# Kernel tuning notes

Measured on AMD Instinct MI355X. Metric: run time of the kernel, lower is better.

The kernel has to match this reference:

```python
import jax, jax.numpy as jnp
import numpy as np

B, L, D, H = 64, 1024, 2048, 128
BUDGET = 10       # args.ceg_budget
STEP = 0.01       # args.ceg_step_size
EPS = 0.2         # _pgd_search default eps


def setup_inputs() -> dict:
    key = jax.random.key(0)
    k0, k1, k2 = jax.random.split(key, 3)
    x = jax.random.normal(k0, (B, L, D), dtype=jnp.float32)
    W1 = jax.random.normal(k1, (D, H), dtype=jnp.float32) * (1.0 / np.sqrt(D))
    b1 = jnp.zeros((H,), dtype=jnp.float32)
    W2 = jax.random.normal(k2, (H, 1), dtype=jnp.float32) * (1.0 / np.sqrt(H))
    b2 = jnp.zeros((1,), dtype=jnp.float32)
    return {"x": x, "W1": W1, "b1": b1, "W2": W2, "b2": b2}


def _score(xa, W1, b1, W2, b2):
    # property_scorer: Linear -> GELU(exact erf, torch default) -> Linear -> Sigmoid
    h = jax.nn.gelu(xa @ W1 + b1, approximate=False)   # [B, H]
    return jax.nn.sigmoid(h @ W2 + b2)                  # [B, 1]


def reference(x, W1, b1, W2, b2):
    pooled = x.mean(axis=1)                             # [B, D]
    # x_adv = pooled + randn * 0.01 (fixed key for determinism)
    noise = jax.random.normal(jax.random.key(1), pooled.shape, pooled.dtype)
    x_adv0 = pooled + 0.01 * noise

    grad_fn = jax.grad(lambda xa: _score(xa, W1, b1, W2, b2).sum())

    def pgd_step(x_adv, _):
        g = jnp.sign(grad_fn(x_adv))
        x_adv = x_adv - STEP * g
        delta = jnp.clip(x_adv - pooled, -EPS, EPS)
        return pooled + delta, None

    x_adv, _ = jax.lax.scan(pgd_step, x_adv0, None, length=BUDGET)

    worst_score = _score(x_adv, W1, b1, W2, b2).squeeze(-1)  # [B]
    violated = worst_score.min() < 0.1                        # scalar bool
    cert_score = 1.0 - worst_score                            # [B]
    return x, worst_score, cert_score, violated
```

## Files before the change

kernel.cpp:

```cpp
#include <hip/hip_runtime.h>
#include <hip/hip_bf16.h>
#include <stdint.h>

#define DEV __device__ __forceinline__

typedef float f32x4 __attribute__((ext_vector_type(4)));

constexpr int nB = 64;
constexpr int nL = 1024;
constexpr int nD = 2048;
constexpr int nH = 128;

constexpr int NT = 16;
constexpr int LT = nL / NT;

constexpr size_t X_ELEMS = (size_t)nB * (size_t)nL * (size_t)nD;

DEV float gelu_f(float x) {
  return 0.5f * x * (1.0f + erff(x * 0.7071067811865476f));
}
DEV float gelu_grad_f(float x) {
  return 0.5f * (1.0f + erff(x * 0.7071067811865476f))
       + x * 0.3989422804014327f * expf(-0.5f * x * x);
}
DEV float sigmoid_f(float x) { return 1.0f / (1.0f + expf(-x)); }

DEV uint32_t rotl32(uint32_t v, int r) { return (v << r) | (v >> (32 - r)); }

DEV float bf2f(uint16_t u) { return __uint_as_float(((uint32_t)u) << 16); }

DEV void threefry_key01(uint32_t& x0, uint32_t& x1) {
  const uint32_t ks0 = 0u, ks1 = 1u, ks2 = 0x1BD11BDAu ^ 0u ^ 1u;
  x0 += ks0; x1 += ks1;
#define TF_RND(r) { x0 += x1; x1 = rotl32(x1, (r)); x1 ^= x0; }
  TF_RND(13) TF_RND(15) TF_RND(26) TF_RND(6)
  x0 += ks1; x1 += ks2 + 1u;
  TF_RND(17) TF_RND(29) TF_RND(16) TF_RND(24)
  x0 += ks2; x1 += ks0 + 2u;
  TF_RND(13) TF_RND(15) TF_RND(26) TF_RND(6)
  x0 += ks0; x1 += ks1 + 3u;
  TF_RND(17) TF_RND(29) TF_RND(16) TF_RND(24)
  x0 += ks1; x1 += ks2 + 4u;
  TF_RND(13) TF_RND(15) TF_RND(26) TF_RND(6)
  x0 += ks2; x1 += ks0 + 5u;
#undef TF_RND
}

DEV float erfinv_f32(float x) {
  float w = -log1pf(-x * x);
  float p;
  if (w < 5.0f) {
    w -= 2.5f;
    p = 2.81022636e-08f;
    p = fmaf(p, w, 3.43273939e-07f);
    p = fmaf(p, w, -3.5233877e-06f);
    p = fmaf(p, w, -4.39150654e-06f);
    p = fmaf(p, w, 0.00021858087f);
    p = fmaf(p, w, -0.00125372503f);
    p = fmaf(p, w, -0.00417768164f);
    p = fmaf(p, w, 0.246640727f);
    p = fmaf(p, w, 1.50140941f);
  } else {
    w = sqrtf(w) - 3.0f;
    p = -0.000200214257f;
    p = fmaf(p, w, 0.000100950558f);
    p = fmaf(p, w, 0.00134934322f);
    p = fmaf(p, w, -0.00367342844f);
    p = fmaf(p, w, 0.00573950773f);
    p = fmaf(p, w, -0.0076224613f);
    p = fmaf(p, w, 0.00943887047f);
    p = fmaf(p, w, 1.00167406f);
    p = fmaf(p, w, 2.83297682f);
  }
  return p * x;
}

DEV float jax_normal_key1(int i) {
  const uint32_t j = (uint32_t)(i & 0xFFFF);
  uint32_t x0 = j, x1 = j + 65536u;
  threefry_key01(x0, x1);
  const uint32_t bits = (i < 65536) ? x0 : x1;
  const float u01 = __uint_as_float((bits >> 9) | 0x3F800000u) - 1.0f;
  const float lo = __uint_as_float(0xBF7FFFFFu);
  float v = u01 * 2.0f + lo;
  v = fmaxf(lo, v);
  return 1.4142135623730951f * erfinv_f32(v);
}

__global__ __launch_bounds__(256) void k_copy_mean(
    const float* __restrict__ x, float* __restrict__ out,
    float* __restrict__ pmean)
{
  const int blk = blockIdx.x;
  const int t = threadIdx.x;
  const size_t base = (size_t)blk * LT * nD;
  const size_t o0 = (size_t)4 * t;
  const size_t o1 = 1024 + (size_t)4 * t;
  f32x4 a0 = {0.f, 0.f, 0.f, 0.f};
  f32x4 a1 = {0.f, 0.f, 0.f, 0.f};
  for (int l = 0; l < LT; l += 2) {
    const size_t r0 = base + (size_t)l * nD;
    const size_t r1 = r0 + nD;
    const f32x4 v0 = *reinterpret_cast<const f32x4*>(x + r0 + o0);
    const f32x4 v1 = *reinterpret_cast<const f32x4*>(x + r0 + o1);
    const f32x4 u0 = *reinterpret_cast<const f32x4*>(x + r1 + o0);
    const f32x4 u1 = *reinterpret_cast<const f32x4*>(x + r1 + o1);
    *reinterpret_cast<f32x4*>(out + r0 + o0) = v0;
    *reinterpret_cast<f32x4*>(out + r0 + o1) = v1;
    *reinterpret_cast<f32x4*>(out + r1 + o0) = u0;
    *reinterpret_cast<f32x4*>(out + r1 + o1) = u1;
    a0 += v0; a1 += v1;
    a0 += u0; a1 += u1;
  }
  float* pm = pmean + (size_t)blk * nD;
  *reinterpret_cast<f32x4*>(pm + o0) = a0;
  *reinterpret_cast<f32x4*>(pm + o1) = a1;
}

__global__ __launch_bounds__(256) void k_copy_mean_atomic(
    const float* __restrict__ x, float* __restrict__ out,
    float* __restrict__ pooled)
{
  const int blk = blockIdx.x;
  const int b = blk >> 4;
  const int t = threadIdx.x;
  const size_t base = (size_t)blk * LT * nD;
  const size_t o0 = (size_t)4 * t;
  const size_t o1 = 1024 + (size_t)4 * t;
  f32x4 a0 = {0.f, 0.f, 0.f, 0.f};
  f32x4 a1 = {0.f, 0.f, 0.f, 0.f};
  for (int l = 0; l < LT; ++l) {
    const size_t r = base + (size_t)l * nD;
    const f32x4 v0 = *reinterpret_cast<const f32x4*>(x + r + o0);
    const f32x4 v1 = *reinterpret_cast<const f32x4*>(x + r + o1);
    *reinterpret_cast<f32x4*>(out + r + o0) = v0;
    *reinterpret_cast<f32x4*>(out + r + o1) = v1;
    a0 += v0; a1 += v1;
  }
  float* pp = pooled + (size_t)b * nD;
  const float sc = 1.0f / nL;
  atomicAdd(&pp[o0+0], a0.x*sc); atomicAdd(&pp[o0+1], a0.y*sc);
  atomicAdd(&pp[o0+2], a0.z*sc); atomicAdd(&pp[o0+3], a0.w*sc);
  atomicAdd(&pp[o1+0], a1.x*sc); atomicAdd(&pp[o1+1], a1.y*sc);
  atomicAdd(&pp[o1+2], a1.z*sc); atomicAdd(&pp[o1+3], a1.w*sc);
}

__global__ __launch_bounds__(256) void k_prep(
    const float* __restrict__ W1, uint16_t* __restrict__ W1b,
    uint16_t* __restrict__ W1Tb)
{
  __shared__ float tile[64][65];
  const int bd = blockIdx.x;
  const int bh = blockIdx.y;
  const int t = threadIdx.x;
  const int j = t & 63;
  const int i0 = (t >> 6) * 16;
  for (int ii = 0; ii < 16; ++ii) {
    const int i = i0 + ii;
    const float v = W1[(size_t)(bd * 64 + i) * nH + bh * 64 + j];
    tile[i][j] = v;
    const __hip_bfloat16 hb = __float2bfloat16(v);
    W1b[(size_t)(bd * 64 + i) * nH + bh * 64 + j] =
        *reinterpret_cast<const uint16_t*>(&hb);
  }
  __syncthreads();
  for (int ii = 0; ii < 16; ++ii) {
    const int i = i0 + ii;
    const __hip_bfloat16 hb = __float2bfloat16(tile[j][i]);
    W1Tb[(size_t)(bh * 64 + i) * nD + bd * 64 + j] =
        *reinterpret_cast<const uint16_t*>(&hb);
  }
}

__global__ __launch_bounds__(1024) void k_pgd(
    const float* __restrict__ W1, const uint16_t* __restrict__ W1b,
    const uint16_t* __restrict__ W1Tb,
    const float* __restrict__ b1, const float* __restrict__ W2,
    const float* __restrict__ b2, const float* __restrict__ pmean,
    const float* __restrict__ pooledG, float* __restrict__ scores,
    const int from_partial)
{
  __shared__ float xaS[nD];
  __shared__ float pooledS[nD];
  __shared__ float redS[16][nH];
  __shared__ float dz1S[nH];
  __shared__ float red2[2];

  const int t = threadIdx.x;
  const int b = blockIdx.x;

  {
    float2 pl;
    if (from_partial) {
      float2 s = make_float2(0.f, 0.f);
      for (int nt2 = 0; nt2 < NT; ++nt2) {
        const float2 v = *reinterpret_cast<const float2*>(
            &pmean[((size_t)(b * NT + nt2)) * nD + 2 * t]);
        s.x += v.x; s.y += v.y;
      }
      pl = make_float2(s.x * (1.0f / nL), s.y * (1.0f / nL));
    } else {
      pl = *reinterpret_cast<const float2*>(&pooledG[(size_t)b * nD + 2 * t]);
    }
    pooledS[2 * t]     = pl.x;
    pooledS[2 * t + 1] = pl.y;
    const int i0 = b * nD + 2 * t;
    xaS[2 * t]     = pl.x + 0.01f * jax_normal_key1(i0);
    xaS[2 * t + 1] = pl.y + 0.01f * jax_normal_key1(i0 + 1);
  }

  const float b1t = (t < nH) ? b1[t] : 0.f;
  const float w2t = (t < nH) ? W2[t] : 0.f;
  const float b2s = b2[0];

  __syncthreads();

  const int hp = t & 63;
  const int q  = t >> 6;
  const uint32_t* __restrict__ w1b2 =
      reinterpret_cast<const uint32_t*>(W1b);
  const uint32_t* __restrict__ w1tb2 =
      reinterpret_cast<const uint32_t*>(W1Tb);
  const int hf = t & (nH - 1);
  const int dq = t >> 7;

  float sig_last = 0.f;
  for (int it = 0; it <= 10; ++it) {
    float z1 = 0.f;
    if (it < 10) {
      float accx = 0.f, accy = 0.f;
      const int dbase = q * 128;
      #pragma unroll 8
      for (int dd = 0; dd < 128; ++dd) {
        const float xv = xaS[dbase + dd];
        const uint32_t w = w1b2[(size_t)(dbase + dd) * 64 + hp];
        accx = fmaf(xv, bf2f((uint16_t)(w & 0xFFFF)), accx);
        accy = fmaf(xv, bf2f((uint16_t)(w >> 16)), accy);
      }
      redS[q][2 * hp]     = accx;
      redS[q][2 * hp + 1] = accy;
      __syncthreads();
      if (t < nH) {
        #pragma unroll
        for (int q2 = 0; q2 < 16; ++q2) z1 += redS[q2][t];
        z1 += b1t;
      }
    } else {
      float acc = 0.f;
      const float* __restrict__ w1p = W1 + (size_t)(dq * 256) * nH + hf;
      #pragma unroll 8
      for (int d = 0; d < 256; ++d)
        acc = fmaf(xaS[dq * 256 + d], w1p[(size_t)d * nH], acc);
      redS[dq][hf] = acc;
      __syncthreads();
      if (t < nH) {
        #pragma unroll
        for (int q2 = 0; q2 < 8; ++q2) z1 += redS[q2][t];
        z1 += b1t;
      }
    }

    if (t < nH) {
      float part = gelu_f(z1) * w2t;
      #pragma unroll
      for (int m = 1; m <= 32; m <<= 1) part += __shfl_xor(part, m, 64);
      if ((t & 63) == 0) red2[t >> 6] = part;
    }
    __syncthreads();

    const float sig = sigmoid_f(red2[0] + red2[1] + b2s);
    if (it == 10) { sig_last = sig; break; }

    if (t < nH) dz1S[t] = sig * (1.f - sig) * w2t * gelu_grad_f(z1);
    __syncthreads();

    float gx = 0.f, gy = 0.f;
    #pragma unroll 8
    for (int h = 0; h < nH; ++h) {
      const float dz = dz1S[h];
      const uint32_t w = w1tb2[(size_t)h * 1024 + t];
      gx = fmaf(dz, bf2f((uint16_t)(w & 0xFFFF)), gx);
      gy = fmaf(dz, bf2f((uint16_t)(w >> 16)), gy);
    }
    const float sg0 = (gx > 0.f) ? 1.f : ((gx < 0.f) ? -1.f : 0.f);
    const float sg1 = (gy > 0.f) ? 1.f : ((gy < 0.f) ? -1.f : 0.f);
    const float p0 = pooledS[2 * t], p1 = pooledS[2 * t + 1];
    float d0 = fminf(fmaxf((xaS[2 * t]     - 0.01f * sg0) - p0, -0.2f), 0.2f);
    float d1 = fminf(fmaxf((xaS[2 * t + 1] - 0.01f * sg1) - p1, -0.2f), 0.2f);
    xaS[2 * t]     = p0 + d0;
    xaS[2 * t + 1] = p1 + d1;
    __syncthreads();
  }

  if (t == 0) scores[b] = sig_last;
}

__global__ __launch_bounds__(256) void k_zero(float* __restrict__ p, int n) {
  const int i = blockIdx.x * 256 + threadIdx.x;
  if (i < n) p[i] = 0.f;
}

__global__ __launch_bounds__(64) void k_finalize(
    const float* __restrict__ scores, float* __restrict__ out)
{
  const int t = threadIdx.x;
  const float s = scores[t];
  out[X_ELEMS + t] = s;
  out[X_ELEMS + nB + t] = 1.0f - s;
  float m = s;
  for (int o = 32; o > 0; o >>= 1) m = fminf(m, __shfl_xor(m, o, 64));
  if (t == 0) out[X_ELEMS + 2 * nB] = (m < 0.1f) ? 1.0f : 0.0f;
}

extern "C" void kernel_launch(void* const* d_in, const int* in_sizes, int n_in,
                              void* d_out, int out_size, void* d_ws, size_t ws_size,
                              hipStream_t stream) {
  const float* x  = (const float*)d_in[0];
  const float* W1 = (const float*)d_in[1];
  const float* b1 = (const float*)d_in[2];
  const float* W2 = (const float*)d_in[3];
  const float* b2 = (const float*)d_in[4];
  float* out = (float*)d_out;
  float* ws = (float*)d_ws;

  constexpr size_t PMEAN_ELEMS  = (size_t)nB * NT * nD;
  constexpr size_t POOLED_ELEMS = (size_t)nB * nD;
  constexpr size_t W1_ELEMS     = (size_t)nD * nH;
  const size_t primary_bytes =
      PMEAN_ELEMS * 4 + W1_ELEMS * 2 * 2 + nB * 4;

  if (ws_size >= primary_bytes) {
    float*    pmean  = ws;
    uint16_t* w1b    = (uint16_t*)(ws + PMEAN_ELEMS);
    uint16_t* w1tb   = w1b + W1_ELEMS;
    float*    scores = (float*)(w1tb + W1_ELEMS);

    k_prep<<<dim3(32, 2), 256, 0, stream>>>(W1, w1b, w1tb);
    k_copy_mean<<<nB * NT, 256, 0, stream>>>(x, out, pmean);
    k_pgd<<<nB, 1024, 0, stream>>>(W1, w1b, w1tb, b1, W2, b2,
                                   pmean, nullptr, scores, 1);
    k_finalize<<<1, 64, 0, stream>>>(scores, out);
  } else {
    float*    pooled = ws;
    uint16_t* w1b    = (uint16_t*)(ws + POOLED_ELEMS);
    uint16_t* w1tb   = w1b + W1_ELEMS;
    float*    scores = (float*)(w1tb + W1_ELEMS);

    k_zero<<<(int)(POOLED_ELEMS + 255) / 256, 256, 0, stream>>>(
        pooled, (int)POOLED_ELEMS);
    k_prep<<<dim3(32, 2), 256, 0, stream>>>(W1, w1b, w1tb);
    k_copy_mean_atomic<<<nB * NT, 256, 0, stream>>>(x, out, pooled);
    k_pgd<<<nB, 1024, 0, stream>>>(W1, w1b, w1tb, b1, W2, b2,
                                   nullptr, pooled, scores, 0);
    k_finalize<<<1, 64, 0, stream>>>(scores, out);
  }
}
```

Baseline: 355.9 us.

## Fuse weight prep into copy kernel, finalize into PGD; widen PGD loads

```diff
diff --git a/kernel.cpp b/kernel.cpp
--- a/kernel.cpp
+++ b/kernel.cpp
@@ -5,6 +5,7 @@
 #define DEV __device__ __forceinline__
 
 typedef float f32x4 __attribute__((ext_vector_type(4)));
+typedef float f32x2 __attribute__((ext_vector_type(2)));
 
 constexpr int nB = 64;
 constexpr int nL = 1024;
@@ -27,7 +28,8 @@
 
 DEV uint32_t rotl32(uint32_t v, int r) { return (v << r) | (v >> (32 - r)); }
 
-DEV float bf2f(uint16_t u) { return __uint_as_float(((uint32_t)u) << 16); }
+DEV float bflo(uint32_t u) { return __uint_as_float(u << 16); }
+DEV float bfhi(uint32_t u) { return __uint_as_float(u & 0xFFFF0000u); }
 
 DEV void threefry_key01(uint32_t& x0, uint32_t& x1) {
   const uint32_t ks0 = 0u, ks1 = 1u, ks2 = 0x1BD11BDAu ^ 0u ^ 1u;
@@ -87,34 +89,247 @@
   return 1.4142135623730951f * erfinv_f32(v);
 }
 
-__global__ __launch_bounds__(256) void k_copy_mean(
+__global__ __launch_bounds__(256) void k_copy_prep(
     const float* __restrict__ x, float* __restrict__ out,
-    float* __restrict__ pmean)
+    float* __restrict__ pmean, const float* __restrict__ W1,
+    uint16_t* __restrict__ W1b, uint16_t* __restrict__ W1Tb,
+    int* __restrict__ ctr)
 {
+  __shared__ float tile[64][65];
+  const int t = threadIdx.x;
+
+  if (blockIdx.x >= (unsigned)(nB * NT)) {
+    const int pb = blockIdx.x - nB * NT;
+    const int bd = pb & 31;
+    const int bh = pb >> 5;
+    if (pb == 0 && t == 0) ctr[0] = 0;
+    const int j = t & 63;
+    const int i0 = (t >> 6) * 16;
+    for (int ii = 0; ii < 16; ++ii) {
+      const int i = i0 + ii;
+      const float v = W1[(size_t)(bd * 64 + i) * nH + bh * 64 + j];
+      tile[i][j] = v;
+      const __hip_bfloat16 hb = __float2bfloat16(v);
+      W1b[(size_t)(bd * 64 + i) * nH + bh * 64 + j] =
+          *reinterpret_cast<const uint16_t*>(&hb);
+    }
+    __syncthreads();
+    for (int ii = 0; ii < 16; ++ii) {
+      const int i = i0 + ii;
+      const __hip_bfloat16 hb = __float2bfloat16(tile[j][i]);
+      W1Tb[(size_t)(bh * 64 + i) * nD + bd * 64 + j] =
+          *reinterpret_cast<const uint16_t*>(&hb);
+    }
+    return;
+  }
+
   const int blk = blockIdx.x;
-  const int t = threadIdx.x;
   const size_t base = (size_t)blk * LT * nD;
   const size_t o0 = (size_t)4 * t;
   const size_t o1 = 1024 + (size_t)4 * t;
   f32x4 a0 = {0.f, 0.f, 0.f, 0.f};
   f32x4 a1 = {0.f, 0.f, 0.f, 0.f};
-  for (int l = 0; l < LT; l += 2) {
+  for (int l = 0; l < LT; l += 4) {
     const size_t r0 = base + (size_t)l * nD;
     const size_t r1 = r0 + nD;
+    const size_t r2 = r1 + nD;
+    const size_t r3 = r2 + nD;
     const f32x4 v0 = *reinterpret_cast<const f32x4*>(x + r0 + o0);
     const f32x4 v1 = *reinterpret_cast<const f32x4*>(x + r0 + o1);
-    const f32x4 u0 = *reinterpret_cast<const f32x4*>(x + r1 + o0);
-    const f32x4 u1 = *reinterpret_cast<const f32x4*>(x + r1 + o1);
+    const f32x4 v2 = *reinterpret_cast<const f32x4*>(x + r1 + o0);
+    const f32x4 v3 = *reinterpret_cast<const f32x4*>(x + r1 + o1);
+    const f32x4 v4 = *reinterpret_cast<const f32x4*>(x + r2 + o0);
+    const f32x4 v5 = *reinterpret_cast<const f32x4*>(x + r2 + o1);
+    const f32x4 v6 = *reinterpret_cast<const f32x4*>(x + r3 + o0);
+    const f32x4 v7 = *reinterpret_cast<const f32x4*>(x + r3 + o1);
     *reinterpret_cast<f32x4*>(out + r0 + o0) = v0;
     *reinterpret_cast<f32x4*>(out + r0 + o1) = v1;
-    *reinterpret_cast<f32x4*>(out + r1 + o0) = u0;
-    *reinterpret_cast<f32x4*>(out + r1 + o1) = u1;
+    *reinterpret_cast<f32x4*>(out + r1 + o0) = v2;
+    *reinterpret_cast<f32x4*>(out + r1 + o1) = v3;
+    *reinterpret_cast<f32x4*>(out + r2 + o0) = v4;
+    *reinterpret_cast<f32x4*>(out + r2 + o1) = v5;
+    *reinterpret_cast<f32x4*>(out + r3 + o0) = v6;
+    *reinterpret_cast<f32x4*>(out + r3 + o1) = v7;
     a0 += v0; a1 += v1;
-    a0 += u0; a1 += u1;
+    a0 += v2; a1 += v3;
+    a0 += v4; a1 += v5;
+    a0 += v6; a1 += v7;
   }
   float* pm = pmean + (size_t)blk * nD;
   *reinterpret_cast<f32x4*>(pm + o0) = a0;
   *reinterpret_cast<f32x4*>(pm + o1) = a1;
+}
+
+__global__ __launch_bounds__(1024) void k_pgd(
+    const float* __restrict__ W1, const uint16_t* __restrict__ W1b,
+    const uint16_t* __restrict__ W1Tb,
+    const float* __restrict__ b1, const float* __restrict__ W2,
+    const float* __restrict__ b2, const float* __restrict__ pmean,
+    const float* __restrict__ pooledG, float* __restrict__ scores,
+    int* __restrict__ ctr, float* __restrict__ out,
+    const int from_partial)
+{
+  __shared__ float xaS[nD];
+  __shared__ float pooledS[nD];
+  __shared__ float redS[32][nH];
+  __shared__ float redB[nD];
+  __shared__ float dz1S[nH];
+  __shared__ float red2[2];
+  __shared__ int lastS;
+
+  const int t = threadIdx.x;
+  const int b = blockIdx.x;
+
+  {
+    float2 pl;
+    if (from_partial) {
+      float2 s = make_float2(0.f, 0.f);
+      for (int nt2 = 0; nt2 < NT; ++nt2) {
+        const float2 v = *reinterpret_cast<const float2*>(
+            &pmean[((size_t)(b * NT + nt2)) * nD + 2 * t]);
+        s.x += v.x; s.y += v.y;
+      }
+      pl = make_float2(s.x * (1.0f / nL), s.y * (1.0f / nL));
+    } else {
+      pl = *reinterpret_cast<const float2*>(&pooledG[(size_t)b * nD + 2 * t]);
+    }
+    pooledS[2 * t]     = pl.x;
+    pooledS[2 * t + 1] = pl.y;
+    const int i0 = b * nD + 2 * t;
+    xaS[2 * t]     = pl.x + 0.01f * jax_normal_key1(i0);
+    xaS[2 * t + 1] = pl.y + 0.01f * jax_normal_key1(i0 + 1);
+  }
+
+  const float b1t = (t < nH) ? b1[t] : 0.f;
+  const float w2t = (t < nH) ? W2[t] : 0.f;
+  const float b2s = b2[0];
+
+  __syncthreads();
+
+  const int hq = t & 31;
+  const int c  = t >> 5;
+  const uint2* __restrict__ w1bq =
+      reinterpret_cast<const uint2*>(W1b);
+  const int dqd = t & 511;
+  const int hh  = t >> 9;
+  const uint2* __restrict__ w1tq =
+      reinterpret_cast<const uint2*>(W1Tb);
+  const int hf  = t & (nH - 1);
+  const int dq8 = t >> 7;
+
+  float sig_last = 0.f;
+  for (int it = 0; it <= 10; ++it) {
+    float z1 = 0.f;
+    if (it < 10) {
+      f32x2 a01 = {0.f, 0.f}, a23 = {0.f, 0.f};
+      const int dbase = c * 64;
+      #pragma unroll 4
+      for (int d4 = 0; d4 < 16; ++d4) {
+        const int d = dbase + d4 * 4;
+        const f32x4 xv4 = *reinterpret_cast<const f32x4*>(&xaS[d]);
+        #pragma unroll
+        for (int k = 0; k < 4; ++k) {
+          const uint2 w = w1bq[(size_t)(d + k) * 32 + hq];
+          const f32x2 wa = {bflo(w.x), bfhi(w.x)};
+          const f32x2 wb = {bflo(w.y), bfhi(w.y)};
+          const float xv = xv4[k];
+          a01 += xv * wa;
+          a23 += xv * wb;
+        }
+      }
+      f32x4* rp = reinterpret_cast<f32x4*>(&redS[c][4 * hq]);
+      *rp = (f32x4){a01.x, a01.y, a23.x, a23.y};
+      __syncthreads();
+      if (t < nH) {
+        #pragma unroll
+        for (int c2 = 0; c2 < 32; ++c2) z1 += redS[c2][t];
+        z1 += b1t;
+      }
+    } else {
+      float acc = 0.f;
+      const float* __restrict__ w1p = W1 + (size_t)(dq8 * 256) * nH + hf;
+      #pragma unroll 8
+      for (int d = 0; d < 256; ++d)
+        acc = fmaf(xaS[dq8 * 256 + d], w1p[(size_t)d * nH], acc);
+      redS[dq8][hf] = acc;
+      __syncthreads();
+      if (t < nH) {
+        #pragma unroll
+        for (int q2 = 0; q2 < 8; ++q2) z1 += redS[q2][t];
+        z1 += b1t;
+      }
+    }
+
+    if (t < nH) {
+      float part = gelu_f(z1) * w2t;
+      #pragma unroll
+      for (int m = 1; m <= 32; m <<= 1) part += __shfl_xor(part, m, 64);
+      if ((t & 63) == 0) red2[t >> 6] = part;
+    }
+    __syncthreads();
+
+    const float sig = sigmoid_f(red2[0] + red2[1] + b2s);
+    if (it == 10) { sig_last = sig; break; }
+
+    if (t < nH) dz1S[t] = sig * (1.f - sig) * w2t * gelu_grad_f(z1);
+    __syncthreads();
+
+    f32x2 g01 = {0.f, 0.f}, g23 = {0.f, 0.f};
+    #pragma unroll 8
+    for (int k = 0; k < 64; ++k) {
+      const int h = hh * 64 + k;
+      const float dz = dz1S[h];
+      const uint2 w = w1tq[(size_t)h * 512 + dqd];
+      const f32x2 wa = {bflo(w.x), bfhi(w.x)};
+      const f32x2 wb = {bflo(w.y), bfhi(w.y)};
+      g01 += dz * wa;
+      g23 += dz * wb;
+    }
+    if (hh == 1)
+      *reinterpret_cast<f32x4*>(&redB[4 * dqd]) =
+          (f32x4){g01.x, g01.y, g23.x, g23.y};
+    __syncthreads();
+    if (hh == 0) {
+      const f32x4 o = *reinterpret_cast<const f32x4*>(&redB[4 * dqd]);
+      const float g[4] = {g01.x + o.x, g01.y + o.y, g23.x + o.z, g23.y + o.w};
+      #pragma unroll
+      for (int i = 0; i < 4; ++i) {
+        const int d = 4 * dqd + i;
+        const float gv = g[i];
+        const float sg = (gv > 0.f) ? 1.f : ((gv < 0.f) ? -1.f : 0.f);
+        const float pl = pooledS[d];
+        float dlt = (xaS[d] - 0.01f * sg) - pl;
+        dlt = fminf(fmaxf(dlt, -0.2f), 0.2f);
+        xaS[d] = pl + dlt;
+      }
+    }
+    __syncthreads();
+  }
+
+  if (t == 0) {
+    scores[b] = sig_last;
+    __threadfence();
+    const int prev = __hip_atomic_fetch_add(ctr, 1, __ATOMIC_ACQ_REL,
+                                            __HIP_MEMORY_SCOPE_AGENT);
+    lastS = (prev == nB - 1) ? 1 : 0;
+  }
+  __syncthreads();
+  if (lastS && t < nB) {
+    const float s = (t == b) ? sig_last
+        : __hip_atomic_load(&scores[t], __ATOMIC_RELAXED,
+                            __HIP_MEMORY_SCOPE_AGENT);
+    out[X_ELEMS + t] = s;
+    out[X_ELEMS + nB + t] = 1.0f - s;
+    float m = s;
+    #pragma unroll
+    for (int o = 32; o > 0; o >>= 1) m = fminf(m, __shfl_xor(m, o, 64));
+    if (t == 0) out[X_ELEMS + 2 * nB] = (m < 0.1f) ? 1.0f : 0.0f;
+  }
+}
+
+__global__ __launch_bounds__(256) void k_zero(float* __restrict__ p, int n) {
+  const int i = blockIdx.x * 256 + threadIdx.x;
+  if (i < n) p[i] = 0.f;
 }
 
 __global__ __launch_bounds__(256) void k_copy_mean_atomic(
@@ -145,14 +360,16 @@
   atomicAdd(&pp[o1+2], a1.z*sc); atomicAdd(&pp[o1+3], a1.w*sc);
 }
 
-__global__ __launch_bounds__(256) void k_prep(
+__global__ __launch_bounds__(256) void k_prep_only(
     const float* __restrict__ W1, uint16_t* __restrict__ W1b,
-    uint16_t* __restrict__ W1Tb)
+    uint16_t* __restrict__ W1Tb, int* __restrict__ ctr)
 {
   __shared__ float tile[64][65];
-  const int bd = blockIdx.x;
-  const int bh = blockIdx.y;
+  const int pb = blockIdx.x;
+  const int bd = pb & 31;
+  const int bh = pb >> 5;
   const int t = threadIdx.x;
+  if (pb == 0 && t == 0) ctr[0] = 0;
   const int j = t & 63;
   const int i0 = (t >> 6) * 16;
   for (int ii = 0; ii < 16; ++ii) {
@@ -170,146 +387,6 @@
     W1Tb[(size_t)(bh * 64 + i) * nD + bd * 64 + j] =
         *reinterpret_cast<const uint16_t*>(&hb);
   }
-}
-
-__global__ __launch_bounds__(1024) void k_pgd(
-    const float* __restrict__ W1, const uint16_t* __restrict__ W1b,
-    const uint16_t* __restrict__ W1Tb,
-    const float* __restrict__ b1, const float* __restrict__ W2,
-    const float* __restrict__ b2, const float* __restrict__ pmean,
-    const float* __restrict__ pooledG, float* __restrict__ scores,
-    const int from_partial)
-{
-  __shared__ float xaS[nD];
-  __shared__ float pooledS[nD];
-  __shared__ float redS[16][nH];
-  __shared__ float dz1S[nH];
-  __shared__ float red2[2];
-
-  const int t = threadIdx.x;
-  const int b = blockIdx.x;
-
-  {
-    float2 pl;
-    if (from_partial) {
-      float2 s = make_float2(0.f, 0.f);
-      for (int nt2 = 0; nt2 < NT; ++nt2) {
-        const float2 v = *reinterpret_cast<const float2*>(
-            &pmean[((size_t)(b * NT + nt2)) * nD + 2 * t]);
-        s.x += v.x; s.y += v.y;
-      }
-      pl = make_float2(s.x * (1.0f / nL), s.y * (1.0f / nL));
-    } else {
-      pl = *reinterpret_cast<const float2*>(&pooledG[(size_t)b * nD + 2 * t]);
-    }
-    pooledS[2 * t]     = pl.x;
-    pooledS[2 * t + 1] = pl.y;
-    const int i0 = b * nD + 2 * t;
-    xaS[2 * t]     = pl.x + 0.01f * jax_normal_key1(i0);
-    xaS[2 * t + 1] = pl.y + 0.01f * jax_normal_key1(i0 + 1);
-  }
-
-  const float b1t = (t < nH) ? b1[t] : 0.f;
-  const float w2t = (t < nH) ? W2[t] : 0.f;
-  const float b2s = b2[0];
-
-  __syncthreads();
-
-  const int hp = t & 63;
-  const int q  = t >> 6;
-  const uint32_t* __restrict__ w1b2 =
-      reinterpret_cast<const uint32_t*>(W1b);
-  const uint32_t* __restrict__ w1tb2 =
-      reinterpret_cast<const uint32_t*>(W1Tb);
-  const int hf = t & (nH - 1);
-  const int dq = t >> 7;
-
-  float sig_last = 0.f;
-  for (int it = 0; it <= 10; ++it) {
-    float z1 = 0.f;
-    if (it < 10) {
-      float accx = 0.f, accy = 0.f;
-      const int dbase = q * 128;
-      #pragma unroll 8
-      for (int dd = 0; dd < 128; ++dd) {
-        const float xv = xaS[dbase + dd];
-        const uint32_t w = w1b2[(size_t)(dbase + dd) * 64 + hp];
-        accx = fmaf(xv, bf2f((uint16_t)(w & 0xFFFF)), accx);
-        accy = fmaf(xv, bf2f((uint16_t)(w >> 16)), accy);
-      }
-      redS[q][2 * hp]     = accx;
-      redS[q][2 * hp + 1] = accy;
-      __syncthreads();
-      if (t < nH) {
-        #pragma unroll
-        for (int q2 = 0; q2 < 16; ++q2) z1 += redS[q2][t];
-        z1 += b1t;
-      }
-    } else {
-      float acc = 0.f;
-      const float* __restrict__ w1p = W1 + (size_t)(dq * 256) * nH + hf;
-      #pragma unroll 8
-      for (int d = 0; d < 256; ++d)
-        acc = fmaf(xaS[dq * 256 + d], w1p[(size_t)d * nH], acc);
-      redS[dq][hf] = acc;
-      __syncthreads();
-      if (t < nH) {
-        #pragma unroll
-        for (int q2 = 0; q2 < 8; ++q2) z1 += redS[q2][t];
-        z1 += b1t;
-      }
-    }
-
-    if (t < nH) {
-      float part = gelu_f(z1) * w2t;
-      #pragma unroll
-      for (int m = 1; m <= 32; m <<= 1) part += __shfl_xor(part, m, 64);
-      if ((t & 63) == 0) red2[t >> 6] = part;
-    }
-    __syncthreads();
-
-    const float sig = sigmoid_f(red2[0] + red2[1] + b2s);
-    if (it == 10) { sig_last = sig; break; }
-
-    if (t < nH) dz1S[t] = sig * (1.f - sig) * w2t * gelu_grad_f(z1);
-    __syncthreads();
-
-    float gx = 0.f, gy = 0.f;
-    #pragma unroll 8
-    for (int h = 0; h < nH; ++h) {
-      const float dz = dz1S[h];
-      const uint32_t w = w1tb2[(size_t)h * 1024 + t];
-      gx = fmaf(dz, bf2f((uint16_t)(w & 0xFFFF)), gx);
-      gy = fmaf(dz, bf2f((uint16_t)(w >> 16)), gy);
-    }
-    const float sg0 = (gx > 0.f) ? 1.f : ((gx < 0.f) ? -1.f : 0.f);
-    const float sg1 = (gy > 0.f) ? 1.f : ((gy < 0.f) ? -1.f : 0.f);
-    const float p0 = pooledS[2 * t], p1 = pooledS[2 * t + 1];
-    float d0 = fminf(fmaxf((xaS[2 * t]     - 0.01f * sg0) - p0, -0.2f), 0.2f);
-    float d1 = fminf(fmaxf((xaS[2 * t + 1] - 0.01f * sg1) - p1, -0.2f), 0.2f);
-    xaS[2 * t]     = p0 + d0;
-    xaS[2 * t + 1] = p1 + d1;
-    __syncthreads();
-  }
-
-  if (t == 0) scores[b] = sig_last;
-}
-
-__global__ __launch_bounds__(256) void k_zero(float* __restrict__ p, int n) {
-  const int i = blockIdx.x * 256 + threadIdx.x;
-  if (i < n) p[i] = 0.f;
-}
-
-__global__ __launch_bounds__(64) void k_finalize(
-    const float* __restrict__ scores, float* __restrict__ out)
-{
-  const int t = threadIdx.x;
-  const float s = scores[t];
-  out[X_ELEMS + t] = s;
-  out[X_ELEMS + nB + t] = 1.0f - s;
-  float m = s;
-  for (int o = 32; o > 0; o >>= 1) m = fminf(m, __shfl_xor(m, o, 64));
-  if (t == 0) out[X_ELEMS + 2 * nB] = (m < 0.1f) ? 1.0f : 0.0f;
 }
 
 extern "C" void kernel_launch(void* const* d_in, const int* in_sizes, int n_in,
@@ -327,31 +404,31 @@
   constexpr size_t POOLED_ELEMS = (size_t)nB * nD;
   constexpr size_t W1_ELEMS     = (size_t)nD * nH;
   const size_t primary_bytes =
-      PMEAN_ELEMS * 4 + W1_ELEMS * 2 * 2 + nB * 4;
+      PMEAN_ELEMS * 4 + W1_ELEMS * 2 * 2 + nB * 4 + 64;
 
   if (ws_size >= primary_bytes) {
     float*    pmean  = ws;
     uint16_t* w1b    = (uint16_t*)(ws + PMEAN_ELEMS);
     uint16_t* w1tb   = w1b + W1_ELEMS;
     float*    scores = (float*)(w1tb + W1_ELEMS);
-
-    k_prep<<<dim3(32, 2), 256, 0, stream>>>(W1, w1b, w1tb);
-    k_copy_mean<<<nB * NT, 256, 0, stream>>>(x, out, pmean);
+    int*      ctr    = (int*)(scores + nB);
+
+    k_copy_prep<<<nB * NT + 64, 256, 0, stream>>>(x, out, pmean, W1,
+                                                  w1b, w1tb, ctr);
     k_pgd<<<nB, 1024, 0, stream>>>(W1, w1b, w1tb, b1, W2, b2,
-                                   pmean, nullptr, scores, 1);
-    k_finalize<<<1, 64, 0, stream>>>(scores, out);
+                                   pmean, nullptr, scores, ctr, out, 1);
   } else {
     float*    pooled = ws;
     uint16_t* w1b    = (uint16_t*)(ws + POOLED_ELEMS);
     uint16_t* w1tb   = w1b + W1_ELEMS;
     float*    scores = (float*)(w1tb + W1_ELEMS);
+    int*      ctr    = (int*)(scores + nB);
 
     k_zero<<<(int)(POOLED_ELEMS + 255) / 256, 256, 0, stream>>>(
         pooled, (int)POOLED_ELEMS);
-    k_prep<<<dim3(32, 2), 256, 0, stream>>>(W1, w1b, w1tb);
+    k_prep_only<<<64, 256, 0, stream>>>(W1, w1b, w1tb, ctr);
     k_copy_mean_atomic<<<nB * NT, 256, 0, stream>>>(x, out, pooled);
     k_pgd<<<nB, 1024, 0, stream>>>(W1, w1b, w1tb, b1, W2, b2,
-                                   nullptr, pooled, scores, 0);
-    k_finalize<<<1, 64, 0, stream>>>(scores, out);
-  }
-}
+                                   nullptr, pooled, scores, ctr, out, 0);
+  }
+}
```

New measurement: 395.6 us. +11.2%, slower.
